# Performance work log

Measured on AMD Instinct MI355X. Metric: run time of the kernel, lower is better.

## Reference

```python
import jax, jax.numpy as jnp
import numpy as np

EPS = 1e-6
NUM_HEADS = 4


def setup_inputs() -> dict:
    key = jax.random.key(0)
    ks = jax.random.split(key, 7)
    B, C, H, W = 4, 128, 64, 64
    x = jax.random.normal(ks[0], (B, C, H, W), dtype=jnp.float32)
    norm_w = jnp.ones((C,), dtype=jnp.float32)
    norm_b = jnp.zeros((C,), dtype=jnp.float32)
    # 1x1 convs stored as [out_ch, in_ch] matrices
    qkv_w = jax.random.normal(ks[1], (3 * C, C), dtype=jnp.float32) / np.sqrt(C)
    qkv_b = jnp.zeros((3 * C,), dtype=jnp.float32)
    proj_w = jax.random.normal(ks[2], (C, C), dtype=jnp.float32) / np.sqrt(C)
    proj_b = jnp.zeros((C,), dtype=jnp.float32)
    return {"x": x, "norm_w": norm_w, "norm_b": norm_b,
            "qkv_w": qkv_w, "qkv_b": qkv_b, "proj_w": proj_w, "proj_b": proj_b}


def reference(x, norm_w, norm_b, qkv_w, qkv_b, proj_w, proj_b):
    B, C, H, W = x.shape
    nh = NUM_HEADS
    dh = C // nh
    N = H * W

    # ChannelLayerNorm: stats over channel dim per spatial position
    mean = jnp.mean(x, axis=1, keepdims=True)
    var = jnp.mean(jnp.square(x - mean), axis=1, keepdims=True)  # unbiased=False
    h = (x - mean) * jax.lax.rsqrt(var + EPS)
    h = h * norm_w[None, :, None, None] + norm_b[None, :, None, None]

    # qkv 1x1 conv -> [B, 3C, H, W]
    qkv = jnp.einsum('oc,bchw->bohw', qkv_w, h) + qkv_b[None, :, None, None]
    qkv = qkv.reshape(B, 3, nh, dh, N)
    q, k, v = qkv[:, 0], qkv[:, 1], qkv[:, 2]  # each [B, nh, dh, N]

    scale = dh ** -0.5
    attn = jnp.einsum('bhcn,bhcm->bhnm', q, k) * scale  # [B, nh, N, N]
    attn = jax.nn.softmax(attn, axis=-1)
    h = jnp.einsum('bhnm,bhcm->bhcn', attn, v)  # [B, nh, dh, N]
    h = h.reshape(B, C, H, W)

    h = jnp.einsum('oc,bchw->bohw', proj_w, h) + proj_b[None, :, None, None]
    return x + h
```

## Files before the change

### kernel.cpp

```cpp
#include <hip/hip_runtime.h>
#include <hip/hip_bf16.h>
#include <math.h>

#define BB 4
#define CC 128
#define NH 4
#define DH 32
#define NN 4096
#define OC3 (3*CC)

typedef __attribute__((ext_vector_type(8))) short short8;
typedef __attribute__((ext_vector_type(4))) short short4v;
typedef __attribute__((ext_vector_type(4))) float float4v;

__device__ inline short f2bf(float f) {
    unsigned u = __builtin_bit_cast(unsigned, f);
    u += 0x7FFF + ((u >> 16) & 1);
    return (short)(u >> 16);
}
__device__ inline unsigned pk2bf(float a, float b) {
    __hip_bfloat162 h = __float22bfloat162_rn(make_float2(a, b));
    unsigned u; __builtin_memcpy(&u, &h, 4);
    return u;
}

#define HS 136
__global__ __launch_bounds__(512, 4) void lnqkv_kernel(
        const float* __restrict__ x, const float* __restrict__ nw,
        const float* __restrict__ nb, const float* __restrict__ qw,
        const float* __restrict__ qbias,
        short* __restrict__ qT, short* __restrict__ kT, short* __restrict__ vv) {
    __shared__ short hT[64 * HS];
    __shared__ float red[16][64];
    __shared__ float mrs[2][64];
    int t = threadIdx.x;
    int n0g = blockIdx.x * 64;
    int b = n0g >> 12, n0 = n0g & (NN - 1);
    int nl = t & 63, cq = t >> 6;

    const float* xp = x + ((size_t)b * CC + cq * 16) * NN + n0 + nl;
    float xv[16];
    float s = 0.f, ss = 0.f;
    #pragma unroll
    for (int j = 0; j < 16; ++j) {
        xv[j] = xp[(size_t)j * NN];
        s += xv[j]; ss += xv[j] * xv[j];
    }
    red[cq][nl] = s; red[cq + 8][nl] = ss;
    __syncthreads();
    if (t < 64) {
        float s8 = 0.f, q8 = 0.f;
        #pragma unroll
        for (int j = 0; j < 8; ++j) { s8 += red[j][t]; q8 += red[j + 8][t]; }
        float mean = s8 * (1.0f / CC);
        float var  = q8 * (1.0f / CC) - mean * mean;
        mrs[0][t] = mean;
        mrs[1][t] = rsqrtf(var + 1e-6f);
    }
    __syncthreads();
    {
        float mean = mrs[0][nl], rsv = mrs[1][nl];
        #pragma unroll
        for (int j = 0; j < 16; j += 8) {
            union { short8 v; unsigned u[4]; } z;
            #pragma unroll
            for (int k = 0; k < 4; ++k) {
                int c = cq * 16 + j + 2 * k;
                float h0 = (xv[j + 2 * k]     - mean) * rsv * nw[c]     + nb[c];
                float h1 = (xv[j + 2 * k + 1] - mean) * rsv * nw[c + 1] + nb[c + 1];
                z.u[k] = pk2bf(h0, h1);
            }
            *(short8*)&hT[nl * HS + cq * 16 + j] = z.v;
        }
    }
    __syncthreads();

    int w = t >> 6, lane = t & 63;
    int lg = lane >> 4, ln = lane & 15;
    int type = blockIdx.y;
    int ow = w * 16;
    const float* wp = qw + (size_t)(type * CC + ow + ln) * CC;
    float4v a0 = {0,0,0,0}, a1 = {0,0,0,0}, a2 = {0,0,0,0}, a3 = {0,0,0,0};
    #pragma unroll
    for (int cs = 0; cs < 4; ++cs) {
        float4 wa = *(const float4*)(wp + cs * 32 + lg * 8);
        float4 wb = *(const float4*)(wp + cs * 32 + lg * 8 + 4);
        union { short8 v; unsigned u[4]; } af;
        af.u[0] = pk2bf(wa.x, wa.y); af.u[1] = pk2bf(wa.z, wa.w);
        af.u[2] = pk2bf(wb.x, wb.y); af.u[3] = pk2bf(wb.z, wb.w);
        const short* hp = &hT[cs * 32 + lg * 8];
        a0 = __builtin_amdgcn_mfma_f32_16x16x32_bf16(af.v, *(const short8*)&hp[(0  + ln) * HS], a0, 0, 0, 0);
        a1 = __builtin_amdgcn_mfma_f32_16x16x32_bf16(af.v, *(const short8*)&hp[(16 + ln) * HS], a1, 0, 0, 0);
        a2 = __builtin_amdgcn_mfma_f32_16x16x32_bf16(af.v, *(const short8*)&hp[(32 + ln) * HS], a2, 0, 0, 0);
        a3 = __builtin_amdgcn_mfma_f32_16x16x32_bf16(af.v, *(const short8*)&hp[(48 + ln) * HS], a3, 0, 0, 0);
    }
    int r0g = type * CC + ow + lg * 4;
    float b0 = qbias[r0g], b1 = qbias[r0g + 1], b2 = qbias[r0g + 2], b3 = qbias[r0g + 3];
    int hh = ow >> 5;
    int cb = ow & 31;
    float4v* accs[4] = {&a0, &a1, &a2, &a3};
    if (type == 0) {
        const float qs = 0.1767766952966369f * 1.4426950408889634f;
        size_t rowbase = (size_t)(b * NH + hh) * NN + n0;
        #pragma unroll
        for (int nsub = 0; nsub < 4; ++nsub) {
            float4v av = *accs[nsub];
            union { short4v v; unsigned u[2]; } z;
            z.u[0] = pk2bf((av.x + b0) * qs, (av.y + b1) * qs);
            z.u[1] = pk2bf((av.z + b2) * qs, (av.w + b3) * qs);
            *(short4v*)&qT[(rowbase + nsub * 16 + ln) * DH + cb + lg * 4] = z.v;
        }
    } else if (type == 1) {
        size_t rowbase = (size_t)(b * NH + hh) * NN + n0;
        #pragma unroll
        for (int nsub = 0; nsub < 4; ++nsub) {
            float4v av = *accs[nsub];
            union { short4v v; unsigned u[2]; } z;
            z.u[0] = pk2bf(av.x + b0, av.y + b1);
            z.u[1] = pk2bf(av.z + b2, av.w + b3);
            *(short4v*)&kT[(rowbase + nsub * 16 + ln) * DH + cb + lg * 4] = z.v;
        }
    } else {
        size_t cbase = (size_t)((b * NH + hh) * DH + cb + lg * 4);
        #pragma unroll
        for (int nsub = 0; nsub < 4; ++nsub) {
            float4v av = *accs[nsub];
            size_t col = (size_t)n0 + nsub * 16 + ln;
            vv[(cbase + 0) * NN + col] = f2bf(av.x + b0);
            vv[(cbase + 1) * NN + col] = f2bf(av.y + b1);
            vv[(cbase + 2) * NN + col] = f2bf(av.z + b2);
            vv[(cbase + 3) * NN + col] = f2bf(av.w + b3);
        }
    }
}

#define PS 72
union __align__(16) FlashSh {
    short pt[8 * 4 * 16 * PS];
    struct { float mo[3][8][64][8]; float ml[3][8][64]; } m;
};
__global__ __launch_bounds__(512, 2) void flash_kernel(
        const short* __restrict__ qT, const short* __restrict__ kT,
        const short* __restrict__ vv, short* __restrict__ aoT) {
    __shared__ FlashSh sh;
    int blk = blockIdx.x;
    int bh = blk >> 5;
    int qb = blk & 31;
    int b = bh >> 2, hh = bh & 3;
    int n0 = qb * 128;
    int t = threadIdx.x, w = t >> 6, lane = t & 63;
    int lg = lane >> 4, ln = lane & 15;
    int qg = w & 1;
    int split = w >> 1;

    const short* kbase = kT + (size_t)bh * NN * DH + lg * 8;
    const short* vb0 = vv + ((size_t)bh * DH + ln) * NN + lg * 8;
    const short* vb1 = vb0 + (size_t)16 * NN;

    short8 qf[4];
    #pragma unroll
    for (int j = 0; j < 4; ++j)
        qf[j] = *(const short8*)&qT[((size_t)bh * NN + n0 + (qg * 4 + j) * 16 + ln) * DH + lg * 8];

    float4v o0[4], o1[4];
    float ls[4];
    #pragma unroll
    for (int j = 0; j < 4; ++j) {
        o0[j] = (float4v){0,0,0,0}; o1[j] = (float4v){0,0,0,0}; ls[j] = 0.f;
    }
    short* ptw = &sh.pt[(w * 4) * 16 * PS];

    int mbeg = split * (NN / 4), mend = mbeg + NN / 4;
    for (int m0 = mbeg; m0 < mend; m0 += 64) {
        const short* kp = kbase + (size_t)m0 * DH;
        short8 k0 = *(const short8*)(kp + (size_t)(ln +  0) * DH);
        short8 k1 = *(const short8*)(kp + (size_t)(ln + 16) * DH);
        short8 k2 = *(const short8*)(kp + (size_t)(ln + 32) * DH);
        short8 k3 = *(const short8*)(kp + (size_t)(ln + 48) * DH);
        short8 v0 = *(const short8*)(vb0 + m0);
        short8 v1 = *(const short8*)(vb0 + m0 + 32);
        short8 v2 = *(const short8*)(vb1 + m0);
        short8 v3 = *(const short8*)(vb1 + m0 + 32);

        #pragma unroll
        for (int j = 0; j < 4; ++j) {
            float4v s0 = {0,0,0,0}, s1 = s0, s2 = s0, s3 = s0;
            s0 = __builtin_amdgcn_mfma_f32_16x16x32_bf16(k0, qf[j], s0, 0, 0, 0);
            s1 = __builtin_amdgcn_mfma_f32_16x16x32_bf16(k1, qf[j], s1, 0, 0, 0);
            s2 = __builtin_amdgcn_mfma_f32_16x16x32_bf16(k2, qf[j], s2, 0, 0, 0);
            s3 = __builtin_amdgcn_mfma_f32_16x16x32_bf16(k3, qf[j], s3, 0, 0, 0);
            short* ptj = ptw + j * 16 * PS;
            float lacc = 0.f;
            float4v* sv[4] = {&s0, &s1, &s2, &s3};
            #pragma unroll
            for (int jj = 0; jj < 4; ++jj) {
                float4v sj = *sv[jj];
                float p0 = __builtin_amdgcn_exp2f(sj.x);
                float p1 = __builtin_amdgcn_exp2f(sj.y);
                float p2 = __builtin_amdgcn_exp2f(sj.z);
                float p3 = __builtin_amdgcn_exp2f(sj.w);
                lacc += (p0 + p1) + (p2 + p3);
                union { short4v v; unsigned u[2]; } z;
                z.u[0] = pk2bf(p0, p1); z.u[1] = pk2bf(p2, p3);
                *(short4v*)&ptj[ln * PS + jj * 16 + lg * 4] = z.v;
            }
            ls[j] += lacc;
        }

        #pragma unroll
        for (int j = 0; j < 4; ++j) {
            short* ptj = ptw + j * 16 * PS;
            short8 pb0 = *(const short8*)&ptj[ln * PS + 0  + lg * 8];
            short8 pb1 = *(const short8*)&ptj[ln * PS + 32 + lg * 8];
            o0[j] = __builtin_amdgcn_mfma_f32_16x16x32_bf16(v0, pb0, o0[j], 0, 0, 0);
            o1[j] = __builtin_amdgcn_mfma_f32_16x16x32_bf16(v2, pb0, o1[j], 0, 0, 0);
            o0[j] = __builtin_amdgcn_mfma_f32_16x16x32_bf16(v1, pb1, o0[j], 0, 0, 0);
            o1[j] = __builtin_amdgcn_mfma_f32_16x16x32_bf16(v3, pb1, o1[j], 0, 0, 0);
        }
    }

    __syncthreads();
    if (split > 0) {
        int si = split - 1;
        #pragma unroll
        for (int j = 0; j < 4; ++j) {
            int tid = qg * 4 + j;
            float* mp = &sh.m.mo[si][tid][lane][0];
            *(float4*)(mp + 0) = make_float4(o0[j].x, o0[j].y, o0[j].z, o0[j].w);
            *(float4*)(mp + 4) = make_float4(o1[j].x, o1[j].y, o1[j].z, o1[j].w);
            sh.m.ml[si][tid][lane] = ls[j];
        }
    }
    __syncthreads();
    if (split == 0) {
        #pragma unroll
        for (int j = 0; j < 4; ++j) {
            int tid = qg * 4 + j;
            #pragma unroll
            for (int si = 0; si < 3; ++si) {
                const float* mp = &sh.m.mo[si][tid][lane][0];
                float4 a0 = *(const float4*)(mp + 0);
                float4 a1 = *(const float4*)(mp + 4);
                o0[j].x += a0.x; o0[j].y += a0.y; o0[j].z += a0.z; o0[j].w += a0.w;
                o1[j].x += a1.x; o1[j].y += a1.y; o1[j].z += a1.z; o1[j].w += a1.w;
                ls[j] += sh.m.ml[si][tid][lane];
            }
            float lt = ls[j];
            lt += __shfl_xor(lt, 16, 64);
            lt += __shfl_xor(lt, 32, 64);
            float inv = 1.0f / lt;
            short* ap = aoT + ((size_t)b * NN + n0 + tid * 16 + ln) * CC + hh * DH;
            union { short4v v; unsigned u[2]; } z;
            z.u[0] = pk2bf(o0[j].x * inv, o0[j].y * inv);
            z.u[1] = pk2bf(o0[j].z * inv, o0[j].w * inv);
            *(short4v*)&ap[lg * 4] = z.v;
            z.u[0] = pk2bf(o1[j].x * inv, o1[j].y * inv);
            z.u[1] = pk2bf(o1[j].z * inv, o1[j].w * inv);
            *(short4v*)&ap[16 + lg * 4] = z.v;
        }
    }
}

__global__ __launch_bounds__(256) void proj_kernel(
        const short* __restrict__ aoT, const float* __restrict__ pw,
        const float* __restrict__ pb, const float* __restrict__ x,
        float* __restrict__ out) {
    int t = threadIdx.x;
    int n0g = blockIdx.x * 64;
    int b = n0g >> 12, n0 = n0g & (NN - 1);
    int o0 = blockIdx.y * 64;
    int wo = t >> 6, lane = t & 63;
    int lg = lane >> 4, ln = lane & 15;
    int ow = o0 + wo * 16;
    const float* wp = pw + (size_t)(ow + ln) * CC;
    const short* ap = aoT + (size_t)n0g * CC + lg * 8;
    float4v a0 = {0,0,0,0}, a1 = {0,0,0,0}, a2 = {0,0,0,0}, a3 = {0,0,0,0};
    #pragma unroll
    for (int cs = 0; cs < 4; ++cs) {
        float4 wa = *(const float4*)(wp + cs * 32 + lg * 8);
        float4 wb = *(const float4*)(wp + cs * 32 + lg * 8 + 4);
        union { short8 v; unsigned u[4]; } af;
        af.u[0] = pk2bf(wa.x, wa.y); af.u[1] = pk2bf(wa.z, wa.w);
        af.u[2] = pk2bf(wb.x, wb.y); af.u[3] = pk2bf(wb.z, wb.w);
        const short* hp = ap + cs * 32;
        a0 = __builtin_amdgcn_mfma_f32_16x16x32_bf16(af.v, *(const short8*)&hp[(size_t)(0  + ln) * CC], a0, 0, 0, 0);
        a1 = __builtin_amdgcn_mfma_f32_16x16x32_bf16(af.v, *(const short8*)&hp[(size_t)(16 + ln) * CC], a1, 0, 0, 0);
        a2 = __builtin_amdgcn_mfma_f32_16x16x32_bf16(af.v, *(const short8*)&hp[(size_t)(32 + ln) * CC], a2, 0, 0, 0);
        a3 = __builtin_amdgcn_mfma_f32_16x16x32_bf16(af.v, *(const short8*)&hp[(size_t)(48 + ln) * CC], a3, 0, 0, 0);
    }
    int r0 = ow + lg * 4;
    float b0 = pb[r0], b1 = pb[r0 + 1], b2 = pb[r0 + 2], b3 = pb[r0 + 3];
    const float* xbase = x   + ((size_t)b * CC + r0) * NN + n0 + ln;
    float*       obase = out + ((size_t)b * CC + r0) * NN + n0 + ln;
    float4v* accs[4] = {&a0, &a1, &a2, &a3};
    #pragma unroll
    for (int nsub = 0; nsub < 4; ++nsub) {
        float4v av = *accs[nsub];
        const float* xp = xbase + nsub * 16;
        float* op = obase + nsub * 16;
        op[(size_t)0 * NN] = av.x + b0 + xp[(size_t)0 * NN];
        op[(size_t)1 * NN] = av.y + b1 + xp[(size_t)1 * NN];
        op[(size_t)2 * NN] = av.z + b2 + xp[(size_t)2 * NN];
        op[(size_t)3 * NN] = av.w + b3 + xp[(size_t)3 * NN];
    }
}

extern "C" void kernel_launch(void* const* d_in, const int* in_sizes, int n_in,
                              void* d_out, int out_size, void* d_ws, size_t ws_size,
                              hipStream_t stream) {
    const float* x    = (const float*)d_in[0];
    const float* nw   = (const float*)d_in[1];
    const float* nb   = (const float*)d_in[2];
    const float* qkvw = (const float*)d_in[3];
    const float* qkvb = (const float*)d_in[4];
    const float* pw   = (const float*)d_in[5];
    const float* pb   = (const float*)d_in[6];
    float* out = (float*)d_out;

    short* qT  = (short*)d_ws;
    short* kT  = qT + (size_t)BB * NH * NN * DH;
    short* vv  = kT + (size_t)BB * NH * NN * DH;
    short* aoT = vv + (size_t)BB * NH * DH * NN;

    lnqkv_kernel<<<dim3(256, 3), 512, 0, stream>>>(x, nw, nb, qkvw, qkvb, qT, kT, vv);
    flash_kernel<<<dim3(512), 512, 0, stream>>>(qT, kT, vv, aoT);
    proj_kernel<<<dim3(256, 2), 256, 0, stream>>>(aoT, pw, pb, x, out);
}
```

Baseline: 145.0 us.

## Compute softmax row sums via MFMA with ones and shrink LDS footprint

The flash kernel now computes the softmax denominator with an extra MFMA that multiplies a vector of bf16 ones by the bf16 probability tile. This replaces the per-element scalar adds and the cross-lane shuffles. The P tile is consumed right after each j iteration, so each wave needs one 16xPS LDS buffer instead of four, and split-partial outputs are stored as bf16, which shrinks shared memory. The cost is two extra MFMAs per j-step and lower precision: the denominator is summed over bf16-rounded probabilities and the partial outputs are rounded to bf16 before the merge.

```diff
diff --git a/kernel.cpp b/kernel.cpp
--- a/kernel.cpp
+++ b/kernel.cpp
@@ -22,6 +22,10 @@
     __hip_bfloat162 h = __float22bfloat162_rn(make_float2(a, b));
     unsigned u; __builtin_memcpy(&u, &h, 4);
     return u;
+}
+__device__ inline float bf2f(short s) {
+    unsigned u = ((unsigned)(unsigned short)s) << 16;
+    return __builtin_bit_cast(float, u);
 }
 
 #define HS 136
@@ -136,8 +140,8 @@
 
 #define PS 72
 union __align__(16) FlashSh {
-    short pt[8 * 4 * 16 * PS];
-    struct { float mo[3][8][64][8]; float ml[3][8][64]; } m;
+    short pt[8 * 16 * PS];
+    struct { short mo[3][8][64][8]; float ml[3][8][64]; } m;
 };
 __global__ __launch_bounds__(512, 2) void flash_kernel(
         const short* __restrict__ qT, const short* __restrict__ kT,
@@ -162,13 +166,16 @@
     for (int j = 0; j < 4; ++j)
         qf[j] = *(const short8*)&qT[((size_t)bh * NN + n0 + (qg * 4 + j) * 16 + ln) * DH + lg * 8];
 
-    float4v o0[4], o1[4];
-    float ls[4];
+    const short onebf = (short)0x3F80;
+    short8 ones = {onebf, onebf, onebf, onebf, onebf, onebf, onebf, onebf};
+
+    float4v o0[4], o1[4], lac[4];
     #pragma unroll
     for (int j = 0; j < 4; ++j) {
-        o0[j] = (float4v){0,0,0,0}; o1[j] = (float4v){0,0,0,0}; ls[j] = 0.f;
-    }
-    short* ptw = &sh.pt[(w * 4) * 16 * PS];
+        o0[j] = (float4v){0,0,0,0}; o1[j] = (float4v){0,0,0,0};
+        lac[j] = (float4v){0,0,0,0};
+    }
+    short* ptw = &sh.pt[w * 16 * PS];
 
     int mbeg = split * (NN / 4), mend = mbeg + NN / 4;
     for (int m0 = mbeg; m0 < mend; m0 += 64) {
@@ -189,8 +196,6 @@
             s1 = __builtin_amdgcn_mfma_f32_16x16x32_bf16(k1, qf[j], s1, 0, 0, 0);
             s2 = __builtin_amdgcn_mfma_f32_16x16x32_bf16(k2, qf[j], s2, 0, 0, 0);
             s3 = __builtin_amdgcn_mfma_f32_16x16x32_bf16(k3, qf[j], s3, 0, 0, 0);
-            short* ptj = ptw + j * 16 * PS;
-            float lacc = 0.f;
             float4v* sv[4] = {&s0, &s1, &s2, &s3};
             #pragma unroll
             for (int jj = 0; jj < 4; ++jj) {
@@ -199,23 +204,18 @@
                 float p1 = __builtin_amdgcn_exp2f(sj.y);
                 float p2 = __builtin_amdgcn_exp2f(sj.z);
                 float p3 = __builtin_amdgcn_exp2f(sj.w);
-                lacc += (p0 + p1) + (p2 + p3);
                 union { short4v v; unsigned u[2]; } z;
                 z.u[0] = pk2bf(p0, p1); z.u[1] = pk2bf(p2, p3);
-                *(short4v*)&ptj[ln * PS + jj * 16 + lg * 4] = z.v;
+                *(short4v*)&ptw[ln * PS + jj * 16 + lg * 4] = z.v;
             }
-            ls[j] += lacc;
-        }
-
-        #pragma unroll
-        for (int j = 0; j < 4; ++j) {
-            short* ptj = ptw + j * 16 * PS;
-            short8 pb0 = *(const short8*)&ptj[ln * PS + 0  + lg * 8];
-            short8 pb1 = *(const short8*)&ptj[ln * PS + 32 + lg * 8];
-            o0[j] = __builtin_amdgcn_mfma_f32_16x16x32_bf16(v0, pb0, o0[j], 0, 0, 0);
-            o1[j] = __builtin_amdgcn_mfma_f32_16x16x32_bf16(v2, pb0, o1[j], 0, 0, 0);
-            o0[j] = __builtin_amdgcn_mfma_f32_16x16x32_bf16(v1, pb1, o0[j], 0, 0, 0);
-            o1[j] = __builtin_amdgcn_mfma_f32_16x16x32_bf16(v3, pb1, o1[j], 0, 0, 0);
+            short8 pb0 = *(const short8*)&ptw[ln * PS + 0  + lg * 8];
+            short8 pb1 = *(const short8*)&ptw[ln * PS + 32 + lg * 8];
+            o0[j]  = __builtin_amdgcn_mfma_f32_16x16x32_bf16(v0, pb0, o0[j], 0, 0, 0);
+            o1[j]  = __builtin_amdgcn_mfma_f32_16x16x32_bf16(v2, pb0, o1[j], 0, 0, 0);
+            lac[j] = __builtin_amdgcn_mfma_f32_16x16x32_bf16(ones, pb0, lac[j], 0, 0, 0);
+            o0[j]  = __builtin_amdgcn_mfma_f32_16x16x32_bf16(v1, pb1, o0[j], 0, 0, 0);
+            o1[j]  = __builtin_amdgcn_mfma_f32_16x16x32_bf16(v3, pb1, o1[j], 0, 0, 0);
+            lac[j] = __builtin_amdgcn_mfma_f32_16x16x32_bf16(ones, pb1, lac[j], 0, 0, 0);
         }
     }
 
@@ -225,10 +225,13 @@
         #pragma unroll
         for (int j = 0; j < 4; ++j) {
             int tid = qg * 4 + j;
-            float* mp = &sh.m.mo[si][tid][lane][0];
-            *(float4*)(mp + 0) = make_float4(o0[j].x, o0[j].y, o0[j].z, o0[j].w);
-            *(float4*)(mp + 4) = make_float4(o1[j].x, o1[j].y, o1[j].z, o1[j].w);
-            sh.m.ml[si][tid][lane] = ls[j];
+            union { short8 v; unsigned u[4]; } z;
+            z.u[0] = pk2bf(o0[j].x, o0[j].y);
+            z.u[1] = pk2bf(o0[j].z, o0[j].w);
+            z.u[2] = pk2bf(o1[j].x, o1[j].y);
+            z.u[3] = pk2bf(o1[j].z, o1[j].w);
+            *(short8*)&sh.m.mo[si][tid][lane][0] = z.v;
+            sh.m.ml[si][tid][lane] = lac[j].x;
         }
     }
     __syncthreads();
@@ -236,18 +239,16 @@
         #pragma unroll
         for (int j = 0; j < 4; ++j) {
             int tid = qg * 4 + j;
+            float lt = lac[j].x;
             #pragma unroll
             for (int si = 0; si < 3; ++si) {
-                const float* mp = &sh.m.mo[si][tid][lane][0];
-                float4 a0 = *(const float4*)(mp + 0);
-                float4 a1 = *(const float4*)(mp + 4);
-                o0[j].x += a0.x; o0[j].y += a0.y; o0[j].z += a0.z; o0[j].w += a0.w;
-                o1[j].x += a1.x; o1[j].y += a1.y; o1[j].z += a1.z; o1[j].w += a1.w;
-                ls[j] += sh.m.ml[si][tid][lane];
+                short8 q = *(const short8*)&sh.m.mo[si][tid][lane][0];
+                o0[j].x += bf2f(q[0]); o0[j].y += bf2f(q[1]);
+                o0[j].z += bf2f(q[2]); o0[j].w += bf2f(q[3]);
+                o1[j].x += bf2f(q[4]); o1[j].y += bf2f(q[5]);
+                o1[j].z += bf2f(q[6]); o1[j].w += bf2f(q[7]);
+                lt += sh.m.ml[si][tid][lane];
             }
-            float lt = ls[j];
-            lt += __shfl_xor(lt, 16, 64);
-            lt += __shfl_xor(lt, 32, 64);
             float inv = 1.0f / lt;
             short* ap = aoT + ((size_t)b * NN + n0 + tid * 16 + ln) * CC + hh * DH;
             union { short4v v; unsigned u[2]; } z;
```

New measurement: 155.5 us. +7.2%, slower.
